# Performance work log

Measured on AMD Instinct MI355X. Metric: run time of the kernel, lower is better.

## Reference

```python
import jax, jax.numpy as jnp
import numpy as np

B, C, H, W = 1, 256, 48, 64
HW = H * W
HIDDEN, CTX = 128, 64
LEVELS, RADIUS = 4, 4
WIN = 2 * RADIUS + 1
P = WIN * WIN                     # 81 lookup points per level
CORR_DIM = P * LEVELS             # 324
TOP_K = 3
ITERS = 4
STEP_ROT, STEP_TRANS = 0.02, 0.02


def _sample_templates():
    # 12 directions x 3 scales + identity = 37 pose perturbations (as in __init__)
    base = [([0,0,0],[1,0,0]),([0,0,0],[-1,0,0]),([0,0,0],[0,1,0]),([0,0,0],[0,-1,0]),
            ([0,0,0],[0,0,1]),([0,0,0],[0,0,-1]),([1,0,0],[0,0,0]),([-1,0,0],[0,0,0]),
            ([0,1,0],[0,0,0]),([0,-1,0],[0,0,0]),([0,0,1],[0,0,0]),([0,0,-1],[0,0,0])]
    scales = np.array([0.25, 1.0, 4.0], np.float32)
    rot = np.repeat(np.array([r for r, _ in base], np.float32), 3, axis=0)
    trs = np.repeat(np.array([t for _, t in base], np.float32), 3, axis=0)
    sc = np.tile(scales, 12)
    axes = rot / np.clip(np.linalg.norm(rot, axis=1, keepdims=True), 1e-8, None)
    ha = STEP_ROT * sc / 2.0
    dq = np.stack([np.cos(ha), axes[:, 0]*np.sin(ha), axes[:, 1]*np.sin(ha), axes[:, 2]*np.sin(ha)], -1)
    dt = trs * (STEP_TRANS * sc[:, None])
    dq = np.concatenate([dq, [[1., 0., 0., 0.]]], 0)
    dt = np.concatenate([dt, [[0., 0., 0.]]], 0)
    return jnp.asarray(dq), jnp.asarray(dt)

DQ, DT = _sample_templates()     # (37,4), (37,3)
N_SAMPLES = DQ.shape[0]


def qmul(q, r):
    w1, x1, y1, z1 = jnp.moveaxis(q, -1, 0)
    w2, x2, y2, z2 = jnp.moveaxis(r, -1, 0)
    return jnp.stack([w1*w2 - x1*x2 - y1*y2 - z1*z2,
                      w1*x2 + x1*w2 + y1*z2 - z1*y2,
                      w1*y2 - x1*z2 + y1*w2 + z1*x2,
                      w1*z2 + x1*y2 - y1*x2 + z1*w2], -1)


def qapply(q, v):
    qv = jnp.concatenate([jnp.zeros(v.shape[:-1] + (1,), v.dtype), v], -1)
    qc = q * jnp.array([1., -1., -1., -1.], q.dtype)
    return qmul(qmul(q, qv), qc)[..., 1:]


def quat_to_R(q):
    w, x, y, z = jnp.moveaxis(q, -1, 0)
    R = jnp.stack([1-2*(y*y+z*z), 2*(x*y-w*z), 2*(x*z+w*y),
                   2*(x*y+w*z), 1-2*(x*x+z*z), 2*(y*z-w*x),
                   2*(x*z-w*y), 2*(y*z+w*x), 1-2*(x*x+y*y)], -1)
    return R.reshape(q.shape[:-1] + (3, 3))


def conv3(x, w, b):
    y = jax.lax.conv_general_dilated(x, w, (1, 1), 'SAME',
                                     dimension_numbers=('NCHW', 'OIHW', 'NCHW'))
    return y + b[None, :, None, None]


def bilinear_lookup(corr_flat, Hl, Wl, x, y):
    # corr_flat: (B,HW,Hl*Wl); x,y: (B,N,HW,P) -> (B,N,HW,P), zero padding outside
    x0 = jnp.floor(x)
    y0 = jnp.floor(y)
    out = jnp.zeros(x.shape, corr_flat.dtype)
    def gather(idx):
        g = lambda ix: jnp.take_along_axis(corr_flat, ix, axis=-1)
        return jax.vmap(g, in_axes=1, out_axes=1)(idx)   # vmap over N, no corr copy
    for dx_, dy_ in ((0, 0), (1, 0), (0, 1), (1, 1)):
        xi = x0 + dx_
        yi = y0 + dy_
        wgt = (1 - jnp.abs(x - xi)) * (1 - jnp.abs(y - yi))
        valid = (xi >= 0) & (xi < Wl) & (yi >= 0) & (yi < Hl)
        idx = (jnp.clip(yi, 0, Hl - 1) * Wl + jnp.clip(xi, 0, Wl - 1)).astype(jnp.int32)
        out = out + jnp.where(valid, wgt, 0.0) * gather(idx)
    return out


def _forward(fmap_rgb, fmap_depth, depth, context, intrinsics,
             Wz, bz, Wr, br, Wq, bq, Wh, bh, Wfc, bfc):
    f32 = jnp.float32
    fx = 60. + 40. * intrinsics[:, 0]
    fy = 60. + 40. * intrinsics[:, 1]
    cx = W / 2. + 4. * (intrinsics[:, 2] - 0.5)
    cy = H / 2. + 4. * (intrinsics[:, 3] - 0.5)
    d = 4.0 + 20.0 * depth                                  # (B,H,W) metric depth

    # 4D correlation pyramid: corr[b,i,:,:] = <fmap_depth pixel i, fmap_rgb>
    fd = fmap_depth.reshape(B, C, HW).transpose(0, 2, 1)    # (B,HW,C)
    corr = jnp.einsum('bic,bchw->bihw', fd, fmap_rgb) / jnp.sqrt(f32(C))
    pyramid = []
    cl, Hl, Wl = corr, H, W
    for _ in range(LEVELS):
        pyramid.append((cl.reshape(B, HW, Hl * Wl), Hl, Wl))
        cl = cl.reshape(B, HW, Hl // 2, 2, Wl // 2, 2).mean(axis=(3, 5))
        Hl //= 2
        Wl //= 2

    # back-projected depth points (B,HW,3)
    vv, uu = jnp.meshgrid(jnp.arange(H, dtype=f32), jnp.arange(W, dtype=f32), indexing='ij')
    uu = uu.reshape(HW)
    vv = vv.reshape(HW)
    df = d.reshape(B, HW)
    X = jnp.stack([(uu[None] - cx[:, None]) / fx[:, None] * df,
                   (vv[None] - cy[:, None]) / fy[:, None] * df, df], -1)

    off = jnp.arange(-RADIUS, RADIUS + 1, dtype=f32)
    oy, ox = jnp.meshgrid(off, off, indexing='ij')
    ox = ox.reshape(P)
    oy = oy.reshape(P)

    pose = jnp.tile(jnp.array([1., 0., 0., 0., 0., 0., 0.], f32)[None, :], (B, 1))
    h = jnp.zeros((B, HIDDEN, H, W), f32)

    for _ in range(ITERS):
        qc, tc = pose[:, :4], pose[:, 4:7]
        quats = qmul(qc[:, None, :], DQ[None])              # (B,N,4)
        quats = quats / jnp.linalg.norm(quats, axis=-1, keepdims=True)
        trans = tc[:, None, :] + qapply(qc[:, None, :], DT[None])
        Rm = quat_to_R(quats)                               # (B,N,3,3)
        Xc = jnp.einsum('bnij,bpj->bnpi', Rm, X) + trans[:, :, None, :]
        z = jnp.clip(Xc[..., 2], 0.1, None)
        u = fx[:, None, None] * Xc[..., 0] / z + cx[:, None, None]   # (B,N,HW)
        v = fy[:, None, None] * Xc[..., 1] / z + cy[:, None, None]
        feats = []
        for lvl, (cfl, Hl_, Wl_) in enumerate(pyramid):
            s = f32(2 ** lvl)
            xl = u[..., None] / s + ox
            yl = v[..., None] / s + oy
            feats.append(bilinear_lookup(cfl, Hl_, Wl_, xl, yl))
        cf = jnp.concatenate(feats, -1)                     # (B,N,HW,CORR_DIM)
        conf = cf.mean(axis=(2, 3))                         # (B,N) sample confidence
        topv, topi = jax.lax.top_k(conf, TOP_K)
        wk = jax.nn.softmax(topv, axis=-1)                  # confidence-weighted top-K
        idx = jnp.broadcast_to(topi[:, :, None, None], (B, TOP_K, HW, CORR_DIM))
        sel = jnp.take_along_axis(cf, idx, axis=1)
        fused = (wk[:, :, None, None] * sel).sum(1)         # (B,HW,CORR_DIM)
        fused = fused.transpose(0, 2, 1).reshape(B, CORR_DIM, H, W)

        # ConvGRU update
        x_in = jnp.concatenate([fused, context], 1)
        hx = jnp.concatenate([h, x_in], 1)
        zg = jax.nn.sigmoid(conv3(hx, Wz, bz))
        rg = jax.nn.sigmoid(conv3(hx, Wr, br))
        qg = jnp.tanh(conv3(jnp.concatenate([rg * h, x_in], 1), Wq, bq))
        h = (1 - zg) * h + zg * qg

        # 7D pose delta head + quaternion/Lie-style update
        feat = jax.nn.relu(conv3(h, Wh, bh)).mean(axis=(2, 3))
        delta = 0.01 * (feat @ Wfc + bfc)                   # (B,7)
        dq = jnp.concatenate([1.0 + delta[:, :1], delta[:, 1:4]], -1)
        dq = dq / jnp.linalg.norm(dq, axis=-1, keepdims=True)
        tn = tc + qapply(qc, delta[:, 4:7])
        qn = qmul(qc, dq)
        qn = qn / jnp.linalg.norm(qn, axis=-1, keepdims=True)
        pose = jnp.concatenate([qn, tn], -1)
    return pose


def setup_inputs() -> dict:
    key = jax.random.key(0)
    ks = jax.random.split(key, 12)
    rn = lambda k, shape, s=1.0: s * jax.random.normal(k, shape, jnp.float32)
    Gin = HIDDEN + CORR_DIM + CTX
    sc = 1.0 / np.sqrt(Gin * 9)
    sh = 1.0 / np.sqrt(HIDDEN * 9)
    return {
        'fmap_rgb': rn(ks[0], (B, C, H, W)),
        'fmap_depth': rn(ks[1], (B, C, H, W)),
        'depth': jax.random.uniform(ks[2], (B, H, W), jnp.float32),
        'context': rn(ks[3], (B, CTX, H, W)),
        'intrinsics': jax.random.uniform(ks[4], (B, 4), jnp.float32),
        'Wz': rn(ks[5], (HIDDEN, Gin, 3, 3), sc), 'bz': jnp.zeros((HIDDEN,), jnp.float32),
        'Wr': rn(ks[6], (HIDDEN, Gin, 3, 3), sc), 'br': jnp.zeros((HIDDEN,), jnp.float32),
        'Wq': rn(ks[7], (HIDDEN, Gin, 3, 3), sc), 'bq': jnp.zeros((HIDDEN,), jnp.float32),
        'Wh': rn(ks[8], (HIDDEN, HIDDEN, 3, 3), sh), 'bh': jnp.zeros((HIDDEN,), jnp.float32),
        'Wfc': rn(ks[9], (HIDDEN, 7), 1.0 / np.sqrt(HIDDEN)), 'bfc': jnp.zeros((7,), jnp.float32),
    }


def reference(fmap_rgb, fmap_depth, depth, context, intrinsics,
              Wz, bz, Wr, br, Wq, bq, Wh, bh, Wfc, bfc):
    return _forward(fmap_rgb, fmap_depth, depth, context, intrinsics,
                    Wz, bz, Wr, br, Wq, bq, Wh, bh, Wfc, bfc)
```

## Files before the change

### kernel.cpp

```cpp
#include <hip/hip_runtime.h>
#include <math.h>

constexpr int kH = 48, kW = 64, kHW = 3072, kC = 256;
constexpr int kHidden = 128, kCtx = 64;
constexpr int kP = 81, kCorrDim = 324;
constexpr int kNS = 37, kIters = 4;
constexpr int kGin = kHidden + kCorrDim + kCtx;
constexpr int kCinPad = 544;
constexpr int kStepsBig = 17 * 9;
constexpr int kStepsH = 4 * 9;

constexpr int kSB0 = 0, kSB1 = 4292, kSB2 = 5720, kSB3 = 6292, kSBTot = 6580;
constexpr int kHB0 = 0, kHB1 = 3552, kHB2 = 4560, kHB3 = 4872, kHBTot = 4980;

constexpr size_t U_CORR0 = 0;
constexpr size_t U_CORR1 = U_CORR0 + (size_t)kHW * 3072;
constexpr size_t U_CORR2 = U_CORR1 + (size_t)kHW * 768;
constexpr size_t U_CORR3 = U_CORR2 + (size_t)kHW * 192;
constexpr size_t U_END0  = U_CORR3 + (size_t)kHW * 48;
constexpr size_t F_X     = U_END0 / 2;
constexpr size_t F_H     = F_X + (size_t)kHW * 3;
constexpr size_t F_ZPRE  = F_H + (size_t)kHidden * kHW;
constexpr size_t F_END1  = F_ZPRE + (size_t)kHidden * kHW;
constexpr size_t U_BUFT  = F_END1 * 2;
constexpr size_t U_RHT   = U_BUFT + (size_t)kHW * kCinPad;
constexpr size_t U_PZR   = U_RHT + (size_t)kHW * kHidden;
constexpr size_t U_PQ    = U_PZR + (size_t)kStepsBig * 256 * 32;
constexpr size_t U_PH    = U_PQ + (size_t)kStepsBig * 128 * 32;
constexpr size_t U_END2  = U_PH + (size_t)kStepsH * 128 * 32;
constexpr size_t F_BZR   = (U_END2 + 2) / 2;
constexpr size_t F_CONF  = F_BZR + 256;
constexpr size_t F_TK    = F_CONF + 64;
constexpr size_t F_POSE  = F_TK + 16;
constexpr size_t F_FEAT  = F_POSE + 16;
constexpr size_t F_END3  = F_FEAT + 128;
constexpr size_t U_FDT   = F_END3 * 2;
constexpr size_t U_QT    = U_FDT + (size_t)kHW * kC;
constexpr size_t U_SBOX  = U_FDT;

typedef __attribute__((ext_vector_type(8))) short short8;
typedef __attribute__((ext_vector_type(4))) float f32x4;

__device__ inline unsigned short f2b(float f) {
  unsigned int u = __float_as_uint(f);
  unsigned int r = u + 0x7FFF + ((u >> 16) & 1);
  return (unsigned short)(r >> 16);
}
__device__ inline float b2f(unsigned short u) {
  return __uint_as_float(((unsigned int)u) << 16);
}
__device__ inline int clampi(int v, int lo, int hi) { return min(max(v, lo), hi); }

__constant__ float c_rot[12][3] = {
  {0,0,0},{0,0,0},{0,0,0},{0,0,0},{0,0,0},{0,0,0},
  {1,0,0},{-1,0,0},{0,1,0},{0,-1,0},{0,0,1},{0,0,-1}};
__constant__ float c_trs[12][3] = {
  {1,0,0},{-1,0,0},{0,1,0},{0,-1,0},{0,0,1},{0,0,-1},
  {0,0,0},{0,0,0},{0,0,0},{0,0,0},{0,0,0},{0,0,0}};

__device__ inline void d_qmul(const float* q, const float* r, float* o) {
  o[0] = q[0]*r[0] - q[1]*r[1] - q[2]*r[2] - q[3]*r[3];
  o[1] = q[0]*r[1] + q[1]*r[0] + q[2]*r[3] - q[3]*r[2];
  o[2] = q[0]*r[2] - q[1]*r[3] + q[2]*r[0] + q[3]*r[1];
  o[3] = q[0]*r[3] + q[1]*r[2] - q[2]*r[1] + q[3]*r[0];
}
__device__ inline void d_qapply(const float* q, const float* v, float* o) {
  float a0 = -q[1]*v[0] - q[2]*v[1] - q[3]*v[2];
  float a1 =  q[0]*v[0] + q[2]*v[2] - q[3]*v[1];
  float a2 =  q[0]*v[1] - q[1]*v[2] + q[3]*v[0];
  float a3 =  q[0]*v[2] + q[1]*v[1] - q[2]*v[0];
  o[0] = -a0*q[1] + a1*q[0] - a2*q[3] + a3*q[2];
  o[1] = -a0*q[2] + a1*q[3] + a2*q[0] - a3*q[1];
  o[2] = -a0*q[3] - a1*q[2] + a2*q[1] + a3*q[0];
}
__device__ inline void d_intr(const float* intr, float& fx, float& fy, float& cx, float& cy) {
  fx = 60.f + 40.f*intr[0];
  fy = 60.f + 40.f*intr[1];
  cx = 32.f + 4.f*(intr[2] - 0.5f);
  cy = 24.f + 4.f*(intr[3] - 0.5f);
}
__device__ inline void sample_Rt(int t, const float* __restrict__ pose, float* S) {
  float qc[4] = {pose[0], pose[1], pose[2], pose[3]};
  float tc[3] = {pose[4], pose[5], pose[6]};
  float dq[4], dt[3];
  if (t == 36) {
    dq[0] = 1.f; dq[1] = dq[2] = dq[3] = 0.f;
    dt[0] = dt[1] = dt[2] = 0.f;
  } else {
    int j = t / 3, k = t % 3;
    float sc = (k == 0) ? 0.25f : ((k == 1) ? 1.f : 4.f);
    float rx = c_rot[j][0], ry = c_rot[j][1], rz = c_rot[j][2];
    float nrm = sqrtf(rx*rx + ry*ry + rz*rz);
    float axn = fmaxf(nrm, 1e-8f);
    float ax = rx / axn, ay = ry / axn, az = rz / axn;
    float ha = 0.02f * sc * 0.5f;
    float sh = sinf(ha), ch = cosf(ha);
    dq[0] = ch; dq[1] = ax * sh; dq[2] = ay * sh; dq[3] = az * sh;
    dt[0] = c_trs[j][0] * (0.02f * sc);
    dt[1] = c_trs[j][1] * (0.02f * sc);
    dt[2] = c_trs[j][2] * (0.02f * sc);
  }
  float qn[4];
  d_qmul(qc, dq, qn);
  float inv = 1.f / sqrtf(qn[0]*qn[0] + qn[1]*qn[1] + qn[2]*qn[2] + qn[3]*qn[3]);
  qn[0] *= inv; qn[1] *= inv; qn[2] *= inv; qn[3] *= inv;
  float tr[3];
  d_qapply(qc, dt, tr);
  float w = qn[0], x = qn[1], y = qn[2], z = qn[3];
  S[0] = 1.f - 2.f*(y*y + z*z); S[1] = 2.f*(x*y - w*z);       S[2] = 2.f*(x*z + w*y);
  S[3] = 2.f*(x*y + w*z);       S[4] = 1.f - 2.f*(x*x + z*z); S[5] = 2.f*(y*z - w*x);
  S[6] = 2.f*(x*z - w*y);       S[7] = 2.f*(y*z + w*x);       S[8] = 1.f - 2.f*(x*x + y*y);
  S[9]  = tc[0] + tr[0];
  S[10] = tc[1] + tr[1];
  S[11] = tc[2] + tr[2];
}
__device__ inline void project_uv(const float* S, const float* Xp, const float* intr,
                                  float& u, float& v) {
  float xc0 = S[0]*Xp[0] + S[1]*Xp[1] + S[2]*Xp[2] + S[9];
  float xc1 = S[3]*Xp[0] + S[4]*Xp[1] + S[5]*Xp[2] + S[10];
  float xc2 = S[6]*Xp[0] + S[7]*Xp[1] + S[8]*Xp[2] + S[11];
  float z = fmaxf(xc2, 0.1f);
  float fx, fy, cx, cy;
  d_intr(intr, fx, fy, cx, cy);
  u = fx * xc0 / z + cx;
  v = fy * xc1 / z + cy;
}

__global__ void init_k(const float* __restrict__ ctx, const float* __restrict__ bz,
                       const float* __restrict__ br, const float* __restrict__ depth,
                       const float* __restrict__ intr, float* __restrict__ h,
                       unsigned short* __restrict__ bufT, float* __restrict__ bzr,
                       float* __restrict__ X, float* __restrict__ conf,
                       float* __restrict__ feat, float* __restrict__ pose) {
  int idx = blockIdx.x * blockDim.x + threadIdx.x;
  if (idx < kHidden * kHW) {
    h[idx] = 0.f;
    int p = idx >> 7, c = idx & 127;
    bufT[(size_t)p * kCinPad + c] = 0;
  }
  if (idx < kHW * 92) {
    int p = idx / 92, c = idx % 92;
    unsigned short v = 0;
    if (c < 64) v = f2b(ctx[(size_t)c * kHW + p]);
    bufT[(size_t)p * kCinPad + 452 + c] = v;
  }
  if (idx < kHW) {
    float fx, fy, cx, cy;
    d_intr(intr, fx, fy, cx, cy);
    float d = 4.f + 20.f * depth[idx];
    float u = (float)(idx % kW), v = (float)(idx / kW);
    X[idx*3+0] = (u - cx) / fx * d;
    X[idx*3+1] = (v - cy) / fy * d;
    X[idx*3+2] = d;
  }
  if (idx < 256) bzr[idx] = (idx < 128) ? bz[idx] : br[idx - 128];
  if (idx < 64) conf[idx] = 0.f;
  if (idx < 128) feat[idx] = 0.f;
  if (idx == 0) {
    pose[0] = 1.f;
    for (int j = 1; j < 7; ++j) pose[j] = 0.f;
  }
}

__global__ void pack_k(const float* __restrict__ W0, const float* __restrict__ W1,
                       int ocSplit, int OC, int nsteps, int nchunks, int Cin,
                       unsigned short* __restrict__ P) {
  int idx = blockIdx.x * blockDim.x + threadIdx.x;
  int total = nsteps * OC * 4;
  if (idx >= total) return;
  int g = idx & 3;
  int oc = (idx >> 2) % OC;
  int s = idx / (OC * 4);
  int tap = s / nchunks, cc = s % nchunks;
  union { unsigned short u[8]; uint4 q; } v;
#pragma unroll
  for (int j = 0; j < 8; ++j) {
    int ci = cc * 32 + g * 8 + j;
    float w = 0.f;
    if (ci < Cin)
      w = (oc < ocSplit) ? W0[((size_t)oc * Cin + ci) * 9 + tap]
                         : W1[((size_t)(oc - ocSplit) * Cin + ci) * 9 + tap];
    v.u[j] = f2b(w);
  }
  *(uint4*)&P[(size_t)idx * 8] = v.q;
}

__global__ __launch_bounds__(256) void t_bf16_k(const float* __restrict__ src,
                                                unsigned short* __restrict__ dst) {
  __shared__ float t[64][65];
  const int tid = threadIdx.x;
  const int p0 = blockIdx.x * 64, c0 = blockIdx.y * 64;
  const int tx = tid & 63, ty = tid >> 6;
  for (int cl = ty; cl < 64; cl += 4)
    t[cl][tx] = src[(size_t)(c0 + cl) * kHW + p0 + tx];
  __syncthreads();
  for (int pl = ty; pl < 64; pl += 4)
    dst[(size_t)(p0 + pl) * kC + c0 + tx] = f2b(t[tx][pl]);
}

__global__ __launch_bounds__(256) void corr_mfma_k(const unsigned short* __restrict__ fdT,
                                                   const unsigned short* __restrict__ qT,
                                                   unsigned short* __restrict__ Cg) {
  const int tid = threadIdx.x;
  const int wv = tid >> 6, lane = tid & 63;
  const int m = lane & 15, kg = lane >> 4;
  const int i0 = blockIdx.y * 128 + wv * 32;
  const int q0 = blockIdx.x * 128;

  f32x4 acc[2][8];
#pragma unroll
  for (int t = 0; t < 2; ++t)
#pragma unroll
    for (int u = 0; u < 8; ++u) acc[t][u] = (f32x4){0.f, 0.f, 0.f, 0.f};

#pragma unroll
  for (int kc = 0; kc < 8; ++kc) {
    const int kb = kc * 32 + kg * 8;
    short8 a[2], b[8];
#pragma unroll
    for (int t = 0; t < 2; ++t)
      a[t] = *(const short8*)&fdT[(size_t)(i0 + t * 16 + m) * kC + kb];
#pragma unroll
    for (int u = 0; u < 8; ++u)
      b[u] = *(const short8*)&qT[(size_t)(q0 + u * 16 + m) * kC + kb];
#pragma unroll
    for (int t = 0; t < 2; ++t)
#pragma unroll
      for (int u = 0; u < 8; ++u)
        acc[t][u] = __builtin_amdgcn_mfma_f32_16x16x32_bf16(a[t], b[u], acc[t][u], 0, 0, 0);
  }
  const float S = 0.0625f;
#pragma unroll
  for (int t = 0; t < 2; ++t)
#pragma unroll
    for (int u = 0; u < 8; ++u)
#pragma unroll
      for (int r = 0; r < 4; ++r)
        Cg[(size_t)(i0 + t * 16 + kg * 4 + r) * kHW + q0 + u * 16 + m] = f2b(acc[t][u][r] * S);
}

__global__ void pool2_k(const unsigned short* __restrict__ in,
                        unsigned short* __restrict__ out, int Hi, int Wi) {
  int Ho = Hi / 2, Wo = Wi / 2;
  int total = kHW * Ho * Wo;
  int idx = blockIdx.x * blockDim.x + threadIdx.x;
  if (idx >= total) return;
  int i = idx / (Ho * Wo);
  int r = idx % (Ho * Wo);
  int y = r / Wo, x = r % Wo;
  const unsigned short* p = in + (size_t)i * Hi * Wi;
  float v = 0.25f * (b2f(p[(2*y)*Wi + 2*x]) + b2f(p[(2*y)*Wi + 2*x + 1]) +
                     b2f(p[(2*y+1)*Wi + 2*x]) + b2f(p[(2*y+1)*Wi + 2*x + 1]));
  out[idx] = f2b(v);
}

__global__ __launch_bounds__(256) void boxbuild_k(const unsigned short* __restrict__ corr0,
                                                  const unsigned short* __restrict__ corr1,
                                                  const unsigned short* __restrict__ corr2,
                                                  const unsigned short* __restrict__ corr3,
                                                  unsigned short* __restrict__ Sbox) {
  __shared__ float pyr[4080];
  __shared__ float hb[kHBTot];
  const int i = blockIdx.x;
  const int tid = threadIdx.x;

  for (int idx = tid; idx < 4080; idx += 256) {
    float v;
    if (idx < 3072)      v = b2f(corr0[(size_t)i * 3072 + idx]);
    else if (idx < 3840) v = b2f(corr1[(size_t)i * 768 + idx - 3072]);
    else if (idx < 4032) v = b2f(corr2[(size_t)i * 192 + idx - 3840]);
    else                 v = b2f(corr3[(size_t)i * 48 + idx - 4032]);
    pyr[idx] = v;
  }
  __syncthreads();

  const int lvl_off[4] = {0, 3072, 3840, 4032};
  for (int c = tid; c < kHBTot; c += 256) {
    int lvl, rem;
    if (c < kHB1)      { lvl = 0; rem = c; }
    else if (c < kHB2) { lvl = 1; rem = c - kHB1; }
    else if (c < kHB3) { lvl = 2; rem = c - kHB2; }
    else               { lvl = 3; rem = c - kHB3; }
    const int Wl = kW >> lvl, Wp = Wl + 10;
    const int y = rem / Wp, as = rem % Wp;
    const float* row = &pyr[lvl_off[lvl] + y * Wl];
    const int x0 = max(0, as - 9), x1 = min(Wl - 1, as - 1);
    float s = 0.f;
    for (int x = x0; x <= x1; ++x) s += row[x];
    hb[c] = s;
  }
  __syncthreads();

  const int hoff[4] = {kHB0, kHB1, kHB2, kHB3};
  unsigned short* out = Sbox + (size_t)i * kSBTot;
  for (int c = tid; c < kSBTot; c += 256) {
    int lvl, rem;
    if (c < kSB1)      { lvl = 0; rem = c; }
    else if (c < kSB2) { lvl = 1; rem = c - kSB1; }
    else if (c < kSB3) { lvl = 2; rem = c - kSB2; }
    else               { lvl = 3; rem = c - kSB3; }
    const int Wl = kW >> lvl, Hl = kH >> lvl, Wp = Wl + 10;
    const int bp = rem / Wp, as = rem % Wp;
    const float* col = &hb[hoff[lvl] + as];
    const int r0 = max(0, bp - 9), r1 = min(Hl - 1, bp - 1);
    float s = 0.f;
    for (int r = r0; r <= r1; ++r) s += col[r * Wp];
    out[c] = f2b(s);
  }
}

__global__ __launch_bounds__(256) void conf_k(const unsigned short* __restrict__ Sbox,
                                              const float* __restrict__ X,
                                              const float* __restrict__ pose,
                                              const float* __restrict__ intr,
                                              float* __restrict__ conf) {
  const int idx = blockIdx.x * 256 + threadIdx.x;
  const int n = idx / kHW, i = idx - n * kHW;
  float S[12];
  sample_Rt(n, pose, S);
  float Xp[3] = {X[i*3], X[i*3+1], X[i*3+2]};
  float u, v;
  project_uv(S, Xp, intr, u, v);
  const unsigned short* sb = Sbox + (size_t)i * kSBTot;
  float tot = 0.f;
#pragma unroll
  for (int l = 0; l < 4; ++l) {
    const int Wp = (kW >> l) + 10, Hp = (kH >> l) + 10;
    const int so = (l == 0) ? kSB0 : (l == 1) ? kSB1 : (l == 2) ? kSB2 : kSB3;
    const float s = (float)(1 << l);
    const float bx = u / s, by = v / s;
    const float fbx = floorf(bx), fby = floorf(by);
    const int x0 = (int)fbx, y0 = (int)fby;
    const float fx = bx - fbx, fy = by - fby;
    const int xa = clampi(x0 + 5, 0, Wp - 1), xb = clampi(x0 + 6, 0, Wp - 1);
    const int ya = clampi(y0 + 5, 0, Hp - 1), yb = clampi(y0 + 6, 0, Hp - 1);
    const float s00 = b2f(sb[so + ya * Wp + xa]), s10 = b2f(sb[so + ya * Wp + xb]);
    const float s01 = b2f(sb[so + yb * Wp + xa]), s11 = b2f(sb[so + yb * Wp + xb]);
    tot += (1.f - fx) * (1.f - fy) * s00 + fx * (1.f - fy) * s10 +
           (1.f - fx) * fy * s01 + fx * fy * s11;
  }
#pragma unroll
  for (int o = 32; o; o >>= 1) tot += __shfl_xor(tot, o, 64);
  if ((threadIdx.x & 63) == 0) atomicAdd(&conf[n], tot);
}

__global__ void topk_k(float* __restrict__ conf, float* __restrict__ tkw,
                       int* __restrict__ tki) {
  if (threadIdx.x != 0) return;
  const float scale = 1.f / ((float)kHW * (float)kCorrDim);
  float c[kNS];
  for (int n = 0; n < kNS; ++n) c[n] = conf[n] * scale;
  int id[3] = {-1, -1, -1};
  float v[3];
  for (int k = 0; k < 3; ++k) {
    float best = -1e30f;
    int bi = -1;
    for (int n = 0; n < kNS; ++n) {
      if (n == id[0] || n == id[1] || n == id[2]) continue;
      if (c[n] > best) { best = c[n]; bi = n; }
    }
    v[k] = best;
    id[k] = bi;
  }
  float m = v[0];
  float e0 = expf(v[0] - m), e1 = expf(v[1] - m), e2 = expf(v[2] - m);
  float s = e0 + e1 + e2;
  tkw[0] = e0 / s; tkw[1] = e1 / s; tkw[2] = e2 / s;
  tki[0] = id[0]; tki[1] = id[1]; tki[2] = id[2];
  for (int n = 0; n < kNS; ++n) conf[n] = 0.f;
}

__global__ __launch_bounds__(256) void fused_k(const unsigned short* __restrict__ corr0,
                                               const unsigned short* __restrict__ corr1,
                                               const unsigned short* __restrict__ corr2,
                                               const unsigned short* __restrict__ corr3,
                                               const float* __restrict__ X,
                                               const float* __restrict__ pose,
                                               const float* __restrict__ intr,
                                               const float* __restrict__ tkw,
                                               const int* __restrict__ tki,
                                               unsigned short* __restrict__ bufT) {
  __shared__ float win[12][10][12];
  __shared__ float s_fx[12], s_fy[12];
  __shared__ int   s_ix[12], s_iy[12];
  __shared__ float s_w[3];
  const int i = blockIdx.x;
  const int tid = threadIdx.x;

  if (tid < 3) {
    int n = tki[tid];
    s_w[tid] = tkw[tid];
    float S[12];
    sample_Rt(n, pose, S);
    float Xp[3] = {X[i*3], X[i*3+1], X[i*3+2]};
    float u, v;
    project_uv(S, Xp, intr, u, v);
#pragma unroll
    for (int l = 0; l < 4; ++l) {
      float s = (float)(1 << l);
      float bx = u / s, by = v / s;
      float fbx = floorf(bx), fby = floorf(by);
      s_ix[tid*4 + l] = (int)fbx;
      s_iy[tid*4 + l] = (int)fby;
      s_fx[tid*4 + l] = bx - fbx;
      s_fy[tid*4 + l] = by - fby;
    }
  }
  __syncthreads();

  for (int sidx = tid; sidx < 1200; sidx += 256) {
    const int w = sidx / 100, rem = sidx % 100;
    const int rr = rem / 10, cc = rem % 10;
    const int lvl = w & 3;
    const int Wl = kW >> lvl, Hl = kH >> lvl;
    const unsigned short* base =
        (lvl == 0) ? corr0 : (lvl == 1) ? corr1 : (lvl == 2) ? corr2 : corr3;
    const int y = s_iy[w] - 4 + rr;
    const int x = s_ix[w] - 4 + cc;
    float v = 0.f;
    if (y >= 0 && y < Hl && x >= 0 && x < Wl)
      v = b2f(base[(size_t)i * (Hl * Wl) + y * Wl + x]);
    win[w][rr][cc] = v;
  }
  __syncthreads();

  for (int d = tid; d < kCorrDim; d += 256) {
    const int lvl = d / kP;
    const int o = d % kP;
    const int oyi = o / 9, oxi = o % 9;
    float val = 0.f;
#pragma unroll
    for (int k = 0; k < 3; ++k) {
      const int w = k * 4 + lvl;
      const float fx = s_fx[w], fy = s_fy[w];
      const float w00 = (1.f - fx) * (1.f - fy), w10 = fx * (1.f - fy);
      const float w01 = (1.f - fx) * fy, w11 = fx * fy;
      val += s_w[k] * (w00 * win[w][oyi][oxi] + w10 * win[w][oyi][oxi + 1] +
                       w01 * win[w][oyi + 1][oxi] + w11 * win[w][oyi + 1][oxi + 1]);
    }
    bufT[(size_t)i * kCinPad + kHidden + d] = f2b(val);
  }
}

template<int OC, int NCH, bool QMODE>
__device__ inline void conv_kloop(const unsigned short* __restrict__ inT,
                                  const unsigned short* __restrict__ rhT,
                                  const unsigned short* __restrict__ P,
                                  int y, int wv, int lane, int ocBlock,
                                  f32x4 (&acc)[2][2]) {
  const int m = lane & 15, kg = lane >> 4;
  const int ocW = ocBlock + (wv >> 1) * 32;
  const int pxW = (wv & 1) * 32;
#pragma unroll
  for (int tap = 0; tap < 9; ++tap) {
    const int dy = tap / 3 - 1, dx = tap % 3 - 1;
    const int yy = y + dy;
    if (yy < 0 || yy >= kH) continue;
    const int xs0 = pxW + m + dx, xs1 = pxW + 16 + m + dx;
    const bool v0 = (xs0 >= 0) && (xs0 < kW);
    const bool v1 = (xs1 >= 0) && (xs1 < kW);
    const int px0 = yy * kW + xs0, px1 = yy * kW + xs1;
    const unsigned short* a_base = P + ((size_t)(tap * NCH) * OC + ocW + m) * 32 + kg * 8;
#pragma unroll
    for (int cc = 0; cc < NCH; ++cc) {
      const unsigned short* srcB;
      int stride;
      if (QMODE && cc < 4) { srcB = rhT; stride = kHidden; }
      else                 { srcB = inT; stride = kCinPad; }
      short8 a0 = *(const short8*)(a_base + (size_t)cc * OC * 32);
      short8 a1 = *(const short8*)(a_base + (size_t)cc * OC * 32 + 16 * 32);
      short8 b0 = {0, 0, 0, 0, 0, 0, 0, 0};
      short8 b1 = {0, 0, 0, 0, 0, 0, 0, 0};
      if (v0) b0 = *(const short8*)(srcB + (size_t)px0 * stride + cc * 32 + kg * 8);
      if (v1) b1 = *(const short8*)(srcB + (size_t)px1 * stride + cc * 32 + kg * 8);
      acc[0][0] = __builtin_amdgcn_mfma_f32_16x16x32_bf16(a0, b0, acc[0][0], 0, 0, 0);
      acc[0][1] = __builtin_amdgcn_mfma_f32_16x16x32_bf16(a0, b1, acc[0][1], 0, 0, 0);
      acc[1][0] = __builtin_amdgcn_mfma_f32_16x16x32_bf16(a1, b0, acc[1][0], 0, 0, 0);
      acc[1][1] = __builtin_amdgcn_mfma_f32_16x16x32_bf16(a1, b1, acc[1][1], 0, 0, 0);
    }
  }
}

__global__ __launch_bounds__(256) void conv_zr_k(const unsigned short* __restrict__ bufT,
                                                 const unsigned short* __restrict__ P,
                                                 const float* __restrict__ bzr,
                                                 float* __restrict__ zpre,
                                                 const float* __restrict__ hbuf,
                                                 unsigned short* __restrict__ rhT) {
  const int tid = threadIdx.x;
  const int wv = tid >> 6, lane = tid & 63;
  const int y = blockIdx.y, ocBlock = blockIdx.x * 64;
  f32x4 acc[2][2] = {{{0.f,0.f,0.f,0.f},{0.f,0.f,0.f,0.f}},
                     {{0.f,0.f,0.f,0.f},{0.f,0.f,0.f,0.f}}};
  conv_kloop<256, 17, false>(bufT, nullptr, P, y, wv, lane, ocBlock, acc);
  const int m = lane & 15, kg = lane >> 4;
  const int ocW = ocBlock + (wv >> 1) * 32, pxW = (wv & 1) * 32;
#pragma unroll
  for (int ot = 0; ot < 2; ++ot)
#pragma unroll
    for (int t = 0; t < 2; ++t)
#pragma unroll
      for (int r = 0; r < 4; ++r) {
        const int oc = ocW + ot * 16 + kg * 4 + r;
        const int px = y * kW + pxW + t * 16 + m;
        const float val = acc[ot][t][r] + bzr[oc];
        if (oc < kHidden) {
          zpre[(size_t)oc * kHW + px] = val;
        } else {
          const float rg = 1.f / (1.f + expf(-val));
          rhT[(size_t)px * kHidden + oc - kHidden] = f2b(rg * hbuf[(size_t)(oc - kHidden) * kHW + px]);
        }
      }
}

__global__ __launch_bounds__(256) void conv_q_k(unsigned short* __restrict__ bufT,
                                                const unsigned short* __restrict__ rhT,
                                                const unsigned short* __restrict__ P,
                                                const float* __restrict__ bq,
                                                const float* __restrict__ zpre,
                                                float* __restrict__ hbuf) {
  const int tid = threadIdx.x;
  const int wv = tid >> 6, lane = tid & 63;
  const int y = blockIdx.y, ocBlock = blockIdx.x * 64;
  f32x4 acc[2][2] = {{{0.f,0.f,0.f,0.f},{0.f,0.f,0.f,0.f}},
                     {{0.f,0.f,0.f,0.f},{0.f,0.f,0.f,0.f}}};
  conv_kloop<128, 17, true>(bufT, rhT, P, y, wv, lane, ocBlock, acc);
  const int m = lane & 15, kg = lane >> 4;
  const int ocW = ocBlock + (wv >> 1) * 32, pxW = (wv & 1) * 32;
#pragma unroll
  for (int ot = 0; ot < 2; ++ot)
#pragma unroll
    for (int t = 0; t < 2; ++t)
#pragma unroll
      for (int r = 0; r < 4; ++r) {
        const int oc = ocW + ot * 16 + kg * 4 + r;
        const int px = y * kW + pxW + t * 16 + m;
        const size_t off = (size_t)oc * kHW + px;
        const float q = acc[ot][t][r] + bq[oc];
        const float zg = 1.f / (1.f + expf(-zpre[off]));
        const float hn = (1.f - zg) * hbuf[off] + zg * tanhf(q);
        hbuf[off] = hn;
        bufT[(size_t)px * kCinPad + oc] = f2b(hn);
      }
}

__global__ __launch_bounds__(256) void conv_h_k(const unsigned short* __restrict__ bufT,
                                                const unsigned short* __restrict__ P,
                                                const float* __restrict__ bh,
                                                float* __restrict__ feat) {
  __shared__ float fb[64];
  const int tid = threadIdx.x;
  const int wv = tid >> 6, lane = tid & 63;
  const int y = blockIdx.y, ocBlock = blockIdx.x * 64;
  f32x4 acc[2][2] = {{{0.f,0.f,0.f,0.f},{0.f,0.f,0.f,0.f}},
                     {{0.f,0.f,0.f,0.f},{0.f,0.f,0.f,0.f}}};
  conv_kloop<128, 4, false>(bufT, nullptr, P, y, wv, lane, ocBlock, acc);
  if (tid < 64) fb[tid] = 0.f;
  __syncthreads();
  const int m = lane & 15, kg = lane >> 4;
  const int ocW = ocBlock + (wv >> 1) * 32;
#pragma unroll
  for (int ot = 0; ot < 2; ++ot)
#pragma unroll
    for (int r = 0; r < 4; ++r) {
      const int oc = ocW + ot * 16 + kg * 4 + r;
      const float bv = bh[oc];
      float v = fmaxf(acc[ot][0][r] + bv, 0.f) + fmaxf(acc[ot][1][r] + bv, 0.f);
      v += __shfl_xor(v, 1, 64);
      v += __shfl_xor(v, 2, 64);
      v += __shfl_xor(v, 4, 64);
      v += __shfl_xor(v, 8, 64);
      if (m == 0) atomicAdd(&fb[oc - ocBlock], v);
    }
  __syncthreads();
  if (tid < 64) atomicAdd(&feat[ocBlock + tid], fb[tid]);
}

__global__ void pose_update_k(float* __restrict__ feat, const float* __restrict__ Wfc,
                              const float* __restrict__ bfc, float* __restrict__ pose,
                              float* __restrict__ out) {
  __shared__ float s_d[7];
  int t = threadIdx.x;
  if (t < 7) {
    float s = 0.f;
    const float inv = 1.f / (float)kHW;
    for (int k = 0; k < kHidden; ++k) s += (feat[k] * inv) * Wfc[k * 7 + t];
    s_d[t] = 0.01f * (s + bfc[t]);
  }
  __syncthreads();
  if (t < kHidden) feat[t] = 0.f;
  if (t != 0) return;
  float qc[4] = {pose[0], pose[1], pose[2], pose[3]};
  float tc[3] = {pose[4], pose[5], pose[6]};
  float dq[4] = {1.f + s_d[0], s_d[1], s_d[2], s_d[3]};
  float inv = 1.f / sqrtf(dq[0]*dq[0] + dq[1]*dq[1] + dq[2]*dq[2] + dq[3]*dq[3]);
  dq[0] *= inv; dq[1] *= inv; dq[2] *= inv; dq[3] *= inv;
  float dv[3] = {s_d[4], s_d[5], s_d[6]};
  float rv[3];
  d_qapply(qc, dv, rv);
  float tn[3] = {tc[0] + rv[0], tc[1] + rv[1], tc[2] + rv[2]};
  float qn[4];
  d_qmul(qc, dq, qn);
  float inv2 = 1.f / sqrtf(qn[0]*qn[0] + qn[1]*qn[1] + qn[2]*qn[2] + qn[3]*qn[3]);
  qn[0] *= inv2; qn[1] *= inv2; qn[2] *= inv2; qn[3] *= inv2;
  pose[0] = qn[0]; pose[1] = qn[1]; pose[2] = qn[2]; pose[3] = qn[3];
  pose[4] = tn[0]; pose[5] = tn[1]; pose[6] = tn[2];
  out[0] = qn[0]; out[1] = qn[1]; out[2] = qn[2]; out[3] = qn[3];
  out[4] = tn[0]; out[5] = tn[1]; out[6] = tn[2];
}

extern "C" void kernel_launch(void* const* d_in, const int* in_sizes, int n_in,
                              void* d_out, int out_size, void* d_ws, size_t ws_size,
                              hipStream_t stream) {
  const float* frgb  = (const float*)d_in[0];
  const float* fdep  = (const float*)d_in[1];
  const float* depth = (const float*)d_in[2];
  const float* ctx   = (const float*)d_in[3];
  const float* intr  = (const float*)d_in[4];
  const float* Wz = (const float*)d_in[5];
  const float* bz = (const float*)d_in[6];
  const float* Wr = (const float*)d_in[7];
  const float* br = (const float*)d_in[8];
  const float* Wq = (const float*)d_in[9];
  const float* bq = (const float*)d_in[10];
  const float* Wh = (const float*)d_in[11];
  const float* bh = (const float*)d_in[12];
  const float* Wfc = (const float*)d_in[13];
  const float* bfc = (const float*)d_in[14];
  float* outp = (float*)d_out;

  float* ws = (float*)d_ws;
  unsigned short* us = (unsigned short*)d_ws;
  unsigned short* corr0 = us + U_CORR0;
  unsigned short* corr1 = us + U_CORR1;
  unsigned short* corr2 = us + U_CORR2;
  unsigned short* corr3 = us + U_CORR3;
  float* X    = ws + F_X;
  float* hbuf = ws + F_H;
  float* zpre = ws + F_ZPRE;
  unsigned short* bufT = us + U_BUFT;
  unsigned short* rhT  = us + U_RHT;
  unsigned short* Pzr  = us + U_PZR;
  unsigned short* Pq   = us + U_PQ;
  unsigned short* Ph   = us + U_PH;
  float* bzr  = ws + F_BZR;
  float* conf = ws + F_CONF;
  float* tkw  = ws + F_TK;
  int*   tki  = (int*)(ws + F_TK + 3);
  float* pose = ws + F_POSE;
  float* feat = ws + F_FEAT;
  unsigned short* fdT  = us + U_FDT;
  unsigned short* qT   = us + U_QT;
  unsigned short* Sbox = us + U_SBOX;

  init_k<<<1536, 256, 0, stream>>>(ctx, bz, br, depth, intr, hbuf, bufT, bzr, X,
                                   conf, feat, pose);
  pack_k<<<(kStepsBig * 256 * 4 + 255) / 256, 256, 0, stream>>>(Wz, Wr, 128, 256,
                                                                kStepsBig, 17, kGin, Pzr);
  pack_k<<<(kStepsBig * 128 * 4 + 255) / 256, 256, 0, stream>>>(Wq, Wq, 128, 128,
                                                                kStepsBig, 17, kGin, Pq);
  pack_k<<<(kStepsH * 128 * 4 + 255) / 256, 256, 0, stream>>>(Wh, Wh, 128, 128,
                                                              kStepsH, 4, kHidden, Ph);
  t_bf16_k<<<dim3(48, 4), 256, 0, stream>>>(fdep, fdT);
  t_bf16_k<<<dim3(48, 4), 256, 0, stream>>>(frgb, qT);
  corr_mfma_k<<<dim3(24, 24), 256, 0, stream>>>(fdT, qT, corr0);
  {
    int t1 = kHW * 24 * 32, t2 = kHW * 12 * 16, t3 = kHW * 6 * 8;
    pool2_k<<<(t1 + 255) / 256, 256, 0, stream>>>(corr0, corr1, 48, 64);
    pool2_k<<<(t2 + 255) / 256, 256, 0, stream>>>(corr1, corr2, 24, 32);
    pool2_k<<<(t3 + 255) / 256, 256, 0, stream>>>(corr2, corr3, 12, 16);
  }
  boxbuild_k<<<kHW, 256, 0, stream>>>(corr0, corr1, corr2, corr3, Sbox);

  for (int it = 0; it < kIters; ++it) {
    conf_k<<<444, 256, 0, stream>>>(Sbox, X, pose, intr, conf);
    topk_k<<<1, 64, 0, stream>>>(conf, tkw, tki);
    fused_k<<<kHW, 256, 0, stream>>>(corr0, corr1, corr2, corr3, X, pose, intr,
                                     tkw, tki, bufT);
    conv_zr_k<<<dim3(4, 48), 256, 0, stream>>>(bufT, Pzr, bzr, zpre, hbuf, rhT);
    conv_q_k<<<dim3(2, 48), 256, 0, stream>>>(bufT, rhT, Pq, bq, zpre, hbuf);
    conv_h_k<<<dim3(2, 48), 256, 0, stream>>>(bufT, Ph, bh, feat);
    pose_update_k<<<1, 128, 0, stream>>>(feat, Wfc, bfc, pose, outp);
  }
}
```

Measured before the change: 904.0 us.

## Use prefix sums for box filters and split conv tiles across more blocks

The box-sum precompute now builds row prefix sums with wave scans and column prefix sums per thread. Each window sum then costs two lookups instead of a loop of up to nine adds. The three GRU convolutions also get a smaller per-wave tile: each wave covers 16 output channels by 32 pixels, and the grid doubles to split each row into two halves. This raises block count and occupancy but reloads activation tiles more often, and conv_h now does global atomics directly instead of reducing through shared memory first.

```diff
diff --git a/kernel.cpp b/kernel.cpp
--- a/kernel.cpp
+++ b/kernel.cpp
@@ -254,6 +254,19 @@
   out[idx] = f2b(v);
 }
 
+template<int HL>
+__device__ inline void colpref(float* base, int Wp) {
+  float v[HL];
+#pragma unroll
+  for (int y = 0; y < HL; ++y) v[y] = base[(size_t)y * Wp];
+  float run = 0.f;
+#pragma unroll
+  for (int y = 0; y < HL; ++y) {
+    run += v[y];
+    base[(size_t)y * Wp] = run;
+  }
+}
+
 __global__ __launch_bounds__(256) void boxbuild_k(const unsigned short* __restrict__ corr0,
                                                   const unsigned short* __restrict__ corr1,
                                                   const unsigned short* __restrict__ corr2,
@@ -263,6 +276,7 @@
   __shared__ float hb[kHBTot];
   const int i = blockIdx.x;
   const int tid = threadIdx.x;
+  const int wv = tid >> 6, lane = tid & 63;
 
   for (int idx = tid; idx < 4080; idx += 256) {
     float v;
@@ -275,6 +289,24 @@
   __syncthreads();
 
   const int lvl_off[4] = {0, 3072, 3840, 4032};
+  for (int r = wv; r < 90; r += 4) {
+    int lvl, y;
+    if (r < 48)      { lvl = 0; y = r; }
+    else if (r < 72) { lvl = 1; y = r - 48; }
+    else if (r < 84) { lvl = 2; y = r - 72; }
+    else             { lvl = 3; y = r - 84; }
+    const int Wl = kW >> lvl;
+    float* row = &pyr[lvl_off[lvl] + y * Wl];
+    float v = (lane < Wl) ? row[lane] : 0.f;
+#pragma unroll
+    for (int o = 1; o < 64; o <<= 1) {
+      float tv = __shfl_up(v, o, 64);
+      if (lane >= o) v += tv;
+    }
+    if (lane < Wl) row[lane] = v;
+  }
+  __syncthreads();
+
   for (int c = tid; c < kHBTot; c += 256) {
     int lvl, rem;
     if (c < kHB1)      { lvl = 0; rem = c; }
@@ -283,15 +315,23 @@
     else               { lvl = 3; rem = c - kHB3; }
     const int Wl = kW >> lvl, Wp = Wl + 10;
     const int y = rem / Wp, as = rem % Wp;
-    const float* row = &pyr[lvl_off[lvl] + y * Wl];
-    const int x0 = max(0, as - 9), x1 = min(Wl - 1, as - 1);
-    float s = 0.f;
-    for (int x = x0; x <= x1; ++x) s += row[x];
-    hb[c] = s;
+    const float* pref = &pyr[lvl_off[lvl] + y * Wl];
+    float Hv = 0.f;
+    if (as >= 1) Hv = pref[min(Wl - 1, as - 1)];
+    if (as >= 10) Hv -= pref[as - 10];
+    hb[c] = Hv;
   }
   __syncthreads();
 
   const int hoff[4] = {kHB0, kHB1, kHB2, kHB3};
+  if (tid < 160) {
+    if (tid < 74)       colpref<48>(hb + kHB0 + tid, 74);
+    else if (tid < 116) colpref<24>(hb + kHB1 + (tid - 74), 42);
+    else if (tid < 142) colpref<12>(hb + kHB2 + (tid - 116), 26);
+    else                colpref<6>(hb + kHB3 + (tid - 142), 18);
+  }
+  __syncthreads();
+
   unsigned short* out = Sbox + (size_t)i * kSBTot;
   for (int c = tid; c < kSBTot; c += 256) {
     int lvl, rem;
@@ -302,10 +342,10 @@
     const int Wl = kW >> lvl, Hl = kH >> lvl, Wp = Wl + 10;
     const int bp = rem / Wp, as = rem % Wp;
     const float* col = &hb[hoff[lvl] + as];
-    const int r0 = max(0, bp - 9), r1 = min(Hl - 1, bp - 1);
-    float s = 0.f;
-    for (int r = r0; r <= r1; ++r) s += col[r * Wp];
-    out[c] = f2b(s);
+    float S = 0.f;
+    if (bp >= 1) S = col[(size_t)min(Hl - 1, bp - 1) * Wp];
+    if (bp >= 10) S -= col[(size_t)(bp - 10) * Wp];
+    out[c] = f2b(S);
   }
 }
 
@@ -446,17 +486,16 @@
 __device__ inline void conv_kloop(const unsigned short* __restrict__ inT,
                                   const unsigned short* __restrict__ rhT,
                                   const unsigned short* __restrict__ P,
-                                  int y, int wv, int lane, int ocBlock,
-                                  f32x4 (&acc)[2][2]) {
+                                  int y, int xbase, int wv, int lane, int ocBlock,
+                                  f32x4 (&acc)[2]) {
   const int m = lane & 15, kg = lane >> 4;
-  const int ocW = ocBlock + (wv >> 1) * 32;
-  const int pxW = (wv & 1) * 32;
+  const int ocW = ocBlock + wv * 16;
 #pragma unroll
   for (int tap = 0; tap < 9; ++tap) {
     const int dy = tap / 3 - 1, dx = tap % 3 - 1;
     const int yy = y + dy;
     if (yy < 0 || yy >= kH) continue;
-    const int xs0 = pxW + m + dx, xs1 = pxW + 16 + m + dx;
+    const int xs0 = xbase + m + dx, xs1 = xbase + 16 + m + dx;
     const bool v0 = (xs0 >= 0) && (xs0 < kW);
     const bool v1 = (xs1 >= 0) && (xs1 < kW);
     const int px0 = yy * kW + xs0, px1 = yy * kW + xs1;
@@ -468,15 +507,12 @@
       if (QMODE && cc < 4) { srcB = rhT; stride = kHidden; }
       else                 { srcB = inT; stride = kCinPad; }
       short8 a0 = *(const short8*)(a_base + (size_t)cc * OC * 32);
-      short8 a1 = *(const short8*)(a_base + (size_t)cc * OC * 32 + 16 * 32);
       short8 b0 = {0, 0, 0, 0, 0, 0, 0, 0};
       short8 b1 = {0, 0, 0, 0, 0, 0, 0, 0};
       if (v0) b0 = *(const short8*)(srcB + (size_t)px0 * stride + cc * 32 + kg * 8);
       if (v1) b1 = *(const short8*)(srcB + (size_t)px1 * stride + cc * 32 + kg * 8);
-      acc[0][0] = __builtin_amdgcn_mfma_f32_16x16x32_bf16(a0, b0, acc[0][0], 0, 0, 0);
-      acc[0][1] = __builtin_amdgcn_mfma_f32_16x16x32_bf16(a0, b1, acc[0][1], 0, 0, 0);
-      acc[1][0] = __builtin_amdgcn_mfma_f32_16x16x32_bf16(a1, b0, acc[1][0], 0, 0, 0);
-      acc[1][1] = __builtin_amdgcn_mfma_f32_16x16x32_bf16(a1, b1, acc[1][1], 0, 0, 0);
+      acc[0] = __builtin_amdgcn_mfma_f32_16x16x32_bf16(a0, b0, acc[0], 0, 0, 0);
+      acc[1] = __builtin_amdgcn_mfma_f32_16x16x32_bf16(a0, b1, acc[1], 0, 0, 0);
     }
   }
 }
@@ -489,28 +525,26 @@
                                                  unsigned short* __restrict__ rhT) {
   const int tid = threadIdx.x;
   const int wv = tid >> 6, lane = tid & 63;
-  const int y = blockIdx.y, ocBlock = blockIdx.x * 64;
-  f32x4 acc[2][2] = {{{0.f,0.f,0.f,0.f},{0.f,0.f,0.f,0.f}},
-                     {{0.f,0.f,0.f,0.f},{0.f,0.f,0.f,0.f}}};
-  conv_kloop<256, 17, false>(bufT, nullptr, P, y, wv, lane, ocBlock, acc);
+  const int y = blockIdx.y >> 1, xbase = (blockIdx.y & 1) * 32;
+  const int ocBlock = blockIdx.x * 64;
+  f32x4 acc[2] = {{0.f,0.f,0.f,0.f},{0.f,0.f,0.f,0.f}};
+  conv_kloop<256, 17, false>(bufT, nullptr, P, y, xbase, wv, lane, ocBlock, acc);
   const int m = lane & 15, kg = lane >> 4;
-  const int ocW = ocBlock + (wv >> 1) * 32, pxW = (wv & 1) * 32;
-#pragma unroll
-  for (int ot = 0; ot < 2; ++ot)
-#pragma unroll
-    for (int t = 0; t < 2; ++t)
-#pragma unroll
-      for (int r = 0; r < 4; ++r) {
-        const int oc = ocW + ot * 16 + kg * 4 + r;
-        const int px = y * kW + pxW + t * 16 + m;
-        const float val = acc[ot][t][r] + bzr[oc];
-        if (oc < kHidden) {
-          zpre[(size_t)oc * kHW + px] = val;
-        } else {
-          const float rg = 1.f / (1.f + expf(-val));
-          rhT[(size_t)px * kHidden + oc - kHidden] = f2b(rg * hbuf[(size_t)(oc - kHidden) * kHW + px]);
-        }
+  const int ocW = ocBlock + wv * 16;
+#pragma unroll
+  for (int t = 0; t < 2; ++t)
+#pragma unroll
+    for (int r = 0; r < 4; ++r) {
+      const int oc = ocW + kg * 4 + r;
+      const int px = y * kW + xbase + t * 16 + m;
+      const float val = acc[t][r] + bzr[oc];
+      if (oc < kHidden) {
+        zpre[(size_t)oc * kHW + px] = val;
+      } else {
+        const float rg = 1.f / (1.f + expf(-val));
+        rhT[(size_t)px * kHidden + oc - kHidden] = f2b(rg * hbuf[(size_t)(oc - kHidden) * kHW + px]);
       }
+    }
 }
 
 __global__ __launch_bounds__(256) void conv_q_k(unsigned short* __restrict__ bufT,
@@ -521,59 +555,50 @@
                                                 float* __restrict__ hbuf) {
   const int tid = threadIdx.x;
   const int wv = tid >> 6, lane = tid & 63;
-  const int y = blockIdx.y, ocBlock = blockIdx.x * 64;
-  f32x4 acc[2][2] = {{{0.f,0.f,0.f,0.f},{0.f,0.f,0.f,0.f}},
-                     {{0.f,0.f,0.f,0.f},{0.f,0.f,0.f,0.f}}};
-  conv_kloop<128, 17, true>(bufT, rhT, P, y, wv, lane, ocBlock, acc);
+  const int y = blockIdx.y >> 1, xbase = (blockIdx.y & 1) * 32;
+  const int ocBlock = blockIdx.x * 64;
+  f32x4 acc[2] = {{0.f,0.f,0.f,0.f},{0.f,0.f,0.f,0.f}};
+  conv_kloop<128, 17, true>(bufT, rhT, P, y, xbase, wv, lane, ocBlock, acc);
   const int m = lane & 15, kg = lane >> 4;
-  const int ocW = ocBlock + (wv >> 1) * 32, pxW = (wv & 1) * 32;
-#pragma unroll
-  for (int ot = 0; ot < 2; ++ot)
-#pragma unroll
-    for (int t = 0; t < 2; ++t)
-#pragma unroll
-      for (int r = 0; r < 4; ++r) {
-        const int oc = ocW + ot * 16 + kg * 4 + r;
-        const int px = y * kW + pxW + t * 16 + m;
-        const size_t off = (size_t)oc * kHW + px;
-        const float q = acc[ot][t][r] + bq[oc];
-        const float zg = 1.f / (1.f + expf(-zpre[off]));
-        const float hn = (1.f - zg) * hbuf[off] + zg * tanhf(q);
-        hbuf[off] = hn;
-        bufT[(size_t)px * kCinPad + oc] = f2b(hn);
-      }
+  const int ocW = ocBlock + wv * 16;
+#pragma unroll
+  for (int t = 0; t < 2; ++t)
+#pragma unroll
+    for (int r = 0; r < 4; ++r) {
+      const int oc = ocW + kg * 4 + r;
+      const int px = y * kW + xbase + t * 16 + m;
+      const size_t off = (size_t)oc * kHW + px;
+      const float q = acc[t][r] + bq[oc];
+      const float zg = 1.f / (1.f + expf(-zpre[off]));
+      const float hn = (1.f - zg) * hbuf[off] + zg * tanhf(q);
+      hbuf[off] = hn;
+      bufT[(size_t)px * kCinPad + oc] = f2b(hn);
+    }
 }
 
 __global__ __launch_bounds__(256) void conv_h_k(const unsigned short* __restrict__ bufT,
                                                 const unsigned short* __restrict__ P,
                                                 const float* __restrict__ bh,
                                                 float* __restrict__ feat) {
-  __shared__ float fb[64];
   const int tid = threadIdx.x;
   const int wv = tid >> 6, lane = tid & 63;
-  const int y = blockIdx.y, ocBlock = blockIdx.x * 64;
-  f32x4 acc[2][2] = {{{0.f,0.f,0.f,0.f},{0.f,0.f,0.f,0.f}},
-                     {{0.f,0.f,0.f,0.f},{0.f,0.f,0.f,0.f}}};
-  conv_kloop<128, 4, false>(bufT, nullptr, P, y, wv, lane, ocBlock, acc);
-  if (tid < 64) fb[tid] = 0.f;
-  __syncthreads();
+  const int y = blockIdx.y >> 1, xbase = (blockIdx.y & 1) * 32;
+  const int ocBlock = blockIdx.x * 64;
+  f32x4 acc[2] = {{0.f,0.f,0.f,0.f},{0.f,0.f,0.f,0.f}};
+  conv_kloop<128, 4, false>(bufT, nullptr, P, y, xbase, wv, lane, ocBlock, acc);
   const int m = lane & 15, kg = lane >> 4;
-  const int ocW = ocBlock + (wv >> 1) * 32;
-#pragma unroll
-  for (int ot = 0; ot < 2; ++ot)
-#pragma unroll
-    for (int r = 0; r < 4; ++r) {
-      const int oc = ocW + ot * 16 + kg * 4 + r;
-      const float bv = bh[oc];
-      float v = fmaxf(acc[ot][0][r] + bv, 0.f) + fmaxf(acc[ot][1][r] + bv, 0.f);
-      v += __shfl_xor(v, 1, 64);
-      v += __shfl_xor(v, 2, 64);
-      v += __shfl_xor(v, 4, 64);
-      v += __shfl_xor(v, 8, 64);
-      if (m == 0) atomicAdd(&fb[oc - ocBlock], v);
-    }
-  __syncthreads();
-  if (tid < 64) atomicAdd(&feat[ocBlock + tid], fb[tid]);
+  const int ocW = ocBlock + wv * 16;
+#pragma unroll
+  for (int r = 0; r < 4; ++r) {
+    const int oc = ocW + kg * 4 + r;
+    const float bv = bh[oc];
+    float v = fmaxf(acc[0][r] + bv, 0.f) + fmaxf(acc[1][r] + bv, 0.f);
+    v += __shfl_xor(v, 1, 64);
+    v += __shfl_xor(v, 2, 64);
+    v += __shfl_xor(v, 4, 64);
+    v += __shfl_xor(v, 8, 64);
+    if (m == 0) atomicAdd(&feat[oc], v);
+  }
 }
 
 __global__ void pose_update_k(float* __restrict__ feat, const float* __restrict__ Wfc,
@@ -677,9 +702,9 @@
     topk_k<<<1, 64, 0, stream>>>(conf, tkw, tki);
     fused_k<<<kHW, 256, 0, stream>>>(corr0, corr1, corr2, corr3, X, pose, intr,
                                      tkw, tki, bufT);
-    conv_zr_k<<<dim3(4, 48), 256, 0, stream>>>(bufT, Pzr, bzr, zpre, hbuf, rhT);
-    conv_q_k<<<dim3(2, 48), 256, 0, stream>>>(bufT, rhT, Pq, bq, zpre, hbuf);
-    conv_h_k<<<dim3(2, 48), 256, 0, stream>>>(bufT, Ph, bh, feat);
+    conv_zr_k<<<dim3(4, 96), 256, 0, stream>>>(bufT, Pzr, bzr, zpre, hbuf, rhT);
+    conv_q_k<<<dim3(2, 96), 256, 0, stream>>>(bufT, rhT, Pq, bq, zpre, hbuf);
+    conv_h_k<<<dim3(2, 96), 256, 0, stream>>>(bufT, Ph, bh, feat);
     pose_update_k<<<1, 128, 0, stream>>>(feat, Wfc, bfc, pose, outp);
   }
 }
```

After: 909.8 us. Within noise of the previous version (+0.6%).
